# Kernel tuning notes

Hardware: AMD Instinct MI355X
Metric: run time of the kernel (lower is better)

## Reference

```python
import jax, jax.numpy as jnp
import numpy as np

SLOPE = 25.0   # snntorch surrogate.fast_sigmoid default slope
THR = 1.0      # snntorch Leaky default threshold

@jax.custom_vjp
def spike(x):
    # Heaviside forward, fast-sigmoid surrogate backward: g / (slope*|x|+1)^2
    return (x > 0).astype(x.dtype)

def _spike_fwd(x):
    return spike(x), x

def _spike_bwd(x, g):
    return (g / (SLOPE * jnp.abs(x) + 1.0) ** 2,)

spike.defvjp(_spike_fwd, _spike_bwd)

def _lif(mem, cur, beta):
    # snntorch Leaky, reset_mechanism='subtract':
    # reset computed from previous mem (detached), mem = clamp(beta)*mem + cur - reset*thr
    reset = jax.lax.stop_gradient((mem - THR > 0).astype(mem.dtype))
    mem_new = jnp.clip(beta, 0.0, 1.0) * mem + cur - reset * THR
    spk = spike(mem_new - THR)
    return spk, mem_new

def _dsqn_forward(state_batch, hidden_states, W1, b1, beta1, W2, b2, beta2, W3, b3):
    # state_batch: (B, T, F)
    mem1_0 = hidden_states[:, 0, 0, :]  # (B, 128)
    mem2_0 = hidden_states[:, 0, 1, :]
    # layer1 has no recurrence: precompute all timestep currents at once
    cur1_all = jnp.einsum('btf,hf->bth', state_batch, W1) + b1  # (B, T, 128)
    cur1_all = jnp.swapaxes(cur1_all, 0, 1)                     # (T, B, 128)

    def step(carry, cur1):
        mem1, mem2 = carry
        spk1, mem1 = _lif(mem1, cur1, beta1)
        cur2 = spk1 @ W2.T + b2
        spk2, mem2 = _lif(mem2, cur2, beta2)
        out = spk2 @ W3.T + b3
        return (mem1, mem2), out

    _, outs = jax.lax.scan(step, (mem1_0, mem2_0), cur1_all)  # (T, B, A)
    return jnp.swapaxes(outs, 0, 1)  # (B, T, A)

def setup_inputs() -> dict:
    key = jax.random.key(0)
    ks = jax.random.split(key, 10)
    B, T, F, H, A = 512, 1024, 128, 128, 16
    s = 0.05
    return {
        'state_batch': jax.random.normal(ks[0], (B, T, F), jnp.float32),
        'hidden_states': jnp.zeros((B, 1, 2, H), jnp.float32),
        'W1': jax.random.normal(ks[1], (H, F), jnp.float32) * s,
        'b1': jax.random.normal(ks[2], (H,), jnp.float32) * s,
        'beta1': jax.random.uniform(ks[3], (H,), jnp.float32),
        'W2': jax.random.normal(ks[4], (H, H), jnp.float32) * s,
        'b2': jax.random.normal(ks[5], (H,), jnp.float32) * s,
        'beta2': jax.random.uniform(ks[6], (H,), jnp.float32),
        'W3': jax.random.normal(ks[7], (A, H), jnp.float32) * s,
        'b3': jax.random.normal(ks[8], (A,), jnp.float32) * s,
    }

def reference(state_batch, hidden_states, W1, b1, beta1, W2, b2, beta2, W3, b3):
    return _dsqn_forward(state_batch, hidden_states, W1, b1, beta1, W2, b2, beta2, W3, b3)
```

## Files before the change

kernel.cpp:

```cpp
#include <hip/hip_runtime.h>
#include <cstdint>
#include <cstddef>

#define BB 512
#define TT 1024
#define FF 128
#define HH 128
#define AA 16

#define BAR() asm volatile("s_waitcnt lgkmcnt(0)\n\ts_barrier" ::: "memory")

__device__ __forceinline__ float rl(float v, int l) {
    return __int_as_float(__builtin_amdgcn_readlane(__float_as_int(v), l));
}

__global__ __launch_bounds__(512, 4) void dsqn_fused(
    const float* __restrict__ X,
    const float* __restrict__ hid,
    const float* __restrict__ W1,
    const float* __restrict__ b1,
    const float* __restrict__ beta1,
    const float* __restrict__ W2,
    const float* __restrict__ b2,
    const float* __restrict__ beta2,
    const float* __restrict__ W3,
    const float* __restrict__ b3,
    float* __restrict__ out)
{
    __shared__ float p1b[2][4 * HH];
    __shared__ float p2[2 * HH];
    __shared__ float p3b[2][128];
    __shared__ float w3l[128 * 17];
    __shared__ float obuf[8 * AA];

    const int t = threadIdx.x;
    const int b = blockIdx.x;
    const int lane = t & 63;
    const int wid = t >> 6;
    const bool isC2 = (wid < 4);
    const int u = (wid >> 1) & 1;
    const int q = wid & 3;

    float wA[32], wB[32];
    if (isC2) {
        const float* w2p = W2 + (t & 127) * HH + u * 32;
        #pragma unroll
        for (int k = 0; k < 32; ++k) { wA[k] = w2p[k]; wB[k] = w2p[64 + k]; }
    } else {
        const float* wa = W1 + lane * FF + q;
        const float* wb = W1 + (64 + lane) * FF + q;
        #pragma unroll
        for (int k = 0; k < 32; ++k) { wA[k] = wa[4 * k]; wB[k] = wb[4 * k]; }
    }
    for (int i = t; i < 128 * 16; i += 512) {
        const int r = i >> 4, k = i & 15;
        const int a = r & 15, g = r >> 4;
        w3l[r * 17 + k] = W3[a * HH + g * 16 + k];
    }

    float mem1_0 = hid[b * 2 * HH + lane];
    float mem1_1 = hid[b * 2 * HH + 64 + lane];
    float mem2_0 = hid[b * 2 * HH + HH + lane];
    float mem2_1 = hid[b * 2 * HH + HH + 64 + lane];
    const float b1h0 = b1[lane], b1h1 = b1[64 + lane];
    const float bt1_0 = fminf(fmaxf(beta1[lane], 0.f), 1.f);
    const float bt1_1 = fminf(fmaxf(beta1[64 + lane], 0.f), 1.f);
    const float b2j = b2[t & 127];
    const float bt2_0 = fminf(fmaxf(beta2[lane], 0.f), 1.f);
    const float bt2_1 = fminf(fmaxf(beta2[64 + lane], 0.f), 1.f);
    const float b3a = (t < AA) ? b3[t] : 0.f;

    const float* xrow = X + (size_t)b * TT * FF;
    float* orow = out + (size_t)b * TT * AA;

    const int xidx = 4 * (lane & 31) + q;
    float xv = 0.f;

    if (!isC2) {
        const float xv0 = xrow[xidx];
        float a0 = 0.f, a1 = 0.f;
        #pragma unroll
        for (int k = 0; k < 32; ++k) {
            const float xs = rl(xv0, k);
            a0 = fmaf(xs, wA[k], a0);
            a1 = fmaf(xs, wB[k], a1);
        }
        p1b[0][q * 128 + lane] = a0;
        p1b[0][q * 128 + 64 + lane] = a1;
        xv = xrow[FF + xidx];
    }
    BAR();

    for (int st = 0; st < TT; ++st) {
        const int par = st & 1;

        if (isC2) {
            const float* p1c = p1b[par];
            const float c00 = p1c[lane],       c01 = p1c[128 + lane];
            const float c02 = p1c[256 + lane], c03 = p1c[384 + lane];
            const float c10 = p1c[64 + lane],  c11 = p1c[192 + lane];
            const float c12 = p1c[320 + lane], c13 = p1c[448 + lane];
            const float cur1_0 = ((c00 + c01) + (c02 + c03)) + b1h0;
            const float cur1_1 = ((c10 + c11) + (c12 + c13)) + b1h1;
            const float r1_0 = (mem1_0 > 1.0f) ? 1.0f : 0.0f;
            const float r1_1 = (mem1_1 > 1.0f) ? 1.0f : 0.0f;
            mem1_0 = bt1_0 * mem1_0 + cur1_0 - r1_0;
            mem1_1 = bt1_1 * mem1_1 + cur1_1 - r1_1;
            const unsigned long long balA = __ballot((mem1_0 - 1.0f) > 0.0f);
            const unsigned long long balB = __ballot((mem1_1 - 1.0f) > 0.0f);

            const unsigned wlo = u ? (unsigned)(balA >> 32) : (unsigned)balA;
            const unsigned whi = u ? (unsigned)(balB >> 32) : (unsigned)balB;
            const unsigned long long packed =
                (unsigned long long)wlo | ((unsigned long long)whi << 32);
            const unsigned bit = (unsigned)(packed >> lane) & 1u;
            const float mflt = bit ? 1.0f : 0.0f;

            float c = u ? 0.f : b2j;
            #pragma unroll
            for (int k = 0; k < 32; ++k) c = fmaf(rl(mflt, k), wA[k], c);
            #pragma unroll
            for (int k = 0; k < 32; ++k) c = fmaf(rl(mflt, 32 + k), wB[k], c);
            p2[u * 128 + (t & 127)] = c;
        } else {
            float a0 = 0.f, a1 = 0.f;
            #pragma unroll
            for (int k = 0; k < 32; ++k) {
                const float xs = rl(xv, k);
                a0 = fmaf(xs, wA[k], a0);
                a1 = fmaf(xs, wB[k], a1);
            }
            float* p1n = p1b[par ^ 1];
            p1n[q * 128 + lane] = a0;
            p1n[q * 128 + 64 + lane] = a1;
            xv = (st + 2 < TT) ? xrow[2 * FF + xidx] : 0.f;
            xrow += FF;
        }
        BAR();

        if (isC2) {
            const float cur2_0 = p2[lane] + p2[128 + lane];
            const float cur2_1 = p2[64 + lane] + p2[192 + lane];
            const float r2_0 = (mem2_0 > 1.0f) ? 1.0f : 0.0f;
            const float r2_1 = (mem2_1 > 1.0f) ? 1.0f : 0.0f;
            mem2_0 = bt2_0 * mem2_0 + cur2_0 - r2_0;
            mem2_1 = bt2_1 * mem2_1 + cur2_1 - r2_1;
            const unsigned long long balC = __ballot((mem2_0 - 1.0f) > 0.0f);
            const unsigned long long balD = __ballot((mem2_1 - 1.0f) > 0.0f);

            const int r = t & 127;
            const int g = r >> 4;
            const int wi = r >> 5;
            const unsigned w0m = (unsigned)balC, w1m = (unsigned)(balC >> 32);
            const unsigned w2m = (unsigned)balD, w3m = (unsigned)(balD >> 32);
            const unsigned word = (wi == 0) ? w0m : (wi == 1) ? w1m
                                : (wi == 2) ? w2m : w3m;
            const unsigned chunk = (word >> ((g & 1) * 16)) & 0xFFFFu;
            float p = 0.f;
            #pragma unroll
            for (int k = 0; k < 16; ++k) {
                const float m = __uint_as_float(((chunk >> k) & 1u) * 0x3f800000u);
                p = fmaf(m, w3l[r * 17 + k], p);
            }
            p3b[par][r] = p;
        }
        BAR();

        if (t < AA) {
            float o = b3a;
            #pragma unroll
            for (int gg = 0; gg < 8; ++gg) o += p3b[par][gg * 16 + t];
            obuf[(st & 7) * AA + t] = o;
        }
        if ((st & 7) == 7) {
            BAR();
            if (t < 128) orow[(st - 7) * AA + t] = obuf[t];
        }
    }
}

extern "C" void kernel_launch(void* const* d_in, const int* in_sizes, int n_in,
                              void* d_out, int out_size, void* d_ws, size_t ws_size,
                              hipStream_t stream) {
    const float* X     = (const float*)d_in[0];
    const float* hid   = (const float*)d_in[1];
    const float* W1    = (const float*)d_in[2];
    const float* b1    = (const float*)d_in[3];
    const float* beta1 = (const float*)d_in[4];
    const float* W2    = (const float*)d_in[5];
    const float* b2    = (const float*)d_in[6];
    const float* beta2 = (const float*)d_in[7];
    const float* W3    = (const float*)d_in[8];
    const float* b3    = (const float*)d_in[9];
    float* out = (float*)d_out;

    dsqn_fused<<<BB, 512, 0, stream>>>(X, hid, W1, b1, beta1, W2, b2, beta2, W3, b3, out);
}
```

Measured before the change: 1.718 ms.

## Move layer-3 projection to layer-1 waves, pipelined one step behind, drop barrier

The layer-3 matvec moves from the layer-2 waves to the otherwise idle layer-1 waves. It runs one timestep late, reading spike masks that are published to LDS as four words, and uses W3 held in registers. This removes the third barrier per step and the extra barrier every eighth step. Outputs are now written straight to global memory each step instead of going through an 8-step LDS buffer, and the final step is finished in an epilogue. The cost is more per-step work on the layer-1 waves, more register pressure there, and narrower global stores.

```diff
diff --git a/kernel.cpp b/kernel.cpp
--- a/kernel.cpp
+++ b/kernel.cpp
@@ -9,6 +9,8 @@
 #define AA 16
 
 #define BAR() asm volatile("s_waitcnt lgkmcnt(0)\n\ts_barrier" ::: "memory")
+
+typedef float f32x2 __attribute__((ext_vector_type(2)));
 
 __device__ __forceinline__ float rl(float v, int l) {
     return __int_as_float(__builtin_amdgcn_readlane(__float_as_int(v), l));
@@ -29,9 +31,8 @@
 {
     __shared__ float p1b[2][4 * HH];
     __shared__ float p2[2 * HH];
-    __shared__ float p3b[2][128];
-    __shared__ float w3l[128 * 17];
-    __shared__ float obuf[8 * AA];
+    __shared__ float p3[128];
+    __shared__ unsigned mw2s[4];
 
     const int t = threadIdx.x;
     const int b = blockIdx.x;
@@ -41,40 +42,53 @@
     const int u = (wid >> 1) & 1;
     const int q = wid & 3;
 
-    float wA[32], wB[32];
+    f32x2 wv[32];
+    float w3r[16];
+    int r3 = 0;
     if (isC2) {
         const float* w2p = W2 + (t & 127) * HH + u * 32;
         #pragma unroll
-        for (int k = 0; k < 32; ++k) { wA[k] = w2p[k]; wB[k] = w2p[64 + k]; }
+        for (int k = 0; k < 32; ++k) { wv[k].x = w2p[k]; wv[k].y = w2p[64 + k]; }
     } else {
         const float* wa = W1 + lane * FF + q;
         const float* wb = W1 + (64 + lane) * FF + q;
         #pragma unroll
-        for (int k = 0; k < 32; ++k) { wA[k] = wa[4 * k]; wB[k] = wb[4 * k]; }
-    }
-    for (int i = t; i < 128 * 16; i += 512) {
-        const int r = i >> 4, k = i & 15;
-        const int a = r & 15, g = r >> 4;
-        w3l[r * 17 + k] = W3[a * HH + g * 16 + k];
-    }
-
-    float mem1_0 = hid[b * 2 * HH + lane];
-    float mem1_1 = hid[b * 2 * HH + 64 + lane];
-    float mem2_0 = hid[b * 2 * HH + HH + lane];
-    float mem2_1 = hid[b * 2 * HH + HH + 64 + lane];
-    const float b1h0 = b1[lane], b1h1 = b1[64 + lane];
-    const float bt1_0 = fminf(fmaxf(beta1[lane], 0.f), 1.f);
-    const float bt1_1 = fminf(fmaxf(beta1[64 + lane], 0.f), 1.f);
-    const float b2j = b2[t & 127];
-    const float bt2_0 = fminf(fmaxf(beta2[lane], 0.f), 1.f);
-    const float bt2_1 = fminf(fmaxf(beta2[64 + lane], 0.f), 1.f);
-    const float b3a = (t < AA) ? b3[t] : 0.f;
+        for (int k = 0; k < 32; ++k) { wv[k].x = wa[4 * k]; wv[k].y = wb[4 * k]; }
+        r3 = ((wid & 1) << 6) | lane;
+        const int a3 = r3 & 15, g3 = r3 >> 4;
+        const float* w3p = W3 + a3 * HH + g3 * 16;
+        #pragma unroll
+        for (int k = 0; k < 16; ++k) w3r[k] = w3p[k];
+        #pragma unroll
+        for (int k = 0; k < 16; ++k) asm volatile("" : "+v"(w3r[k]));
+    }
+    #pragma unroll
+    for (int k = 0; k < 32; ++k) asm volatile("" : "+v"(wv[k]));
+
+    float mem1_0 = 0.f, mem1_1 = 0.f, mem2_0 = 0.f, mem2_1 = 0.f;
+    float b1h0 = 0.f, b1h1 = 0.f, bt1_0 = 0.f, bt1_1 = 0.f;
+    float b2j = 0.f, bt2_0 = 0.f, bt2_1 = 0.f;
+    if (isC2) {
+        mem1_0 = hid[b * 2 * HH + lane];
+        mem1_1 = hid[b * 2 * HH + 64 + lane];
+        mem2_0 = hid[b * 2 * HH + HH + lane];
+        mem2_1 = hid[b * 2 * HH + HH + 64 + lane];
+        b1h0 = b1[lane]; b1h1 = b1[64 + lane];
+        bt1_0 = fminf(fmaxf(beta1[lane], 0.f), 1.f);
+        bt1_1 = fminf(fmaxf(beta1[64 + lane], 0.f), 1.f);
+        b2j = b2[t & 127];
+        bt2_0 = fminf(fmaxf(beta2[lane], 0.f), 1.f);
+        bt2_1 = fminf(fmaxf(beta2[64 + lane], 0.f), 1.f);
+    }
+    float b3a = 0.f;
+    if (wid == 4) b3a = b3[lane & 15];
 
     const float* xrow = X + (size_t)b * TT * FF;
     float* orow = out + (size_t)b * TT * AA;
-
     const int xidx = 4 * (lane & 31) + q;
     float xv = 0.f;
+
+    if (t == 0) { mw2s[0] = 0u; mw2s[1] = 0u; mw2s[2] = 0u; mw2s[3] = 0u; }
 
     if (!isC2) {
         const float xv0 = xrow[xidx];
@@ -82,8 +96,8 @@
         #pragma unroll
         for (int k = 0; k < 32; ++k) {
             const float xs = rl(xv0, k);
-            a0 = fmaf(xs, wA[k], a0);
-            a1 = fmaf(xs, wB[k], a1);
+            a0 = fmaf(xs, wv[k].x, a0);
+            a1 = fmaf(xs, wv[k].y, a1);
         }
         p1b[0][q * 128 + lane] = a0;
         p1b[0][q * 128 + 64 + lane] = a1;
@@ -113,26 +127,42 @@
             const unsigned whi = u ? (unsigned)(balB >> 32) : (unsigned)balB;
             const unsigned long long packed =
                 (unsigned long long)wlo | ((unsigned long long)whi << 32);
-            const unsigned bit = (unsigned)(packed >> lane) & 1u;
-            const float mflt = bit ? 1.0f : 0.0f;
+            const float mflt = ((unsigned)(packed >> lane) & 1u) ? 1.0f : 0.0f;
 
             float c = u ? 0.f : b2j;
             #pragma unroll
-            for (int k = 0; k < 32; ++k) c = fmaf(rl(mflt, k), wA[k], c);
-            #pragma unroll
-            for (int k = 0; k < 32; ++k) c = fmaf(rl(mflt, 32 + k), wB[k], c);
+            for (int k = 0; k < 32; ++k) c = fmaf(rl(mflt, k), wv[k].x, c);
+            #pragma unroll
+            for (int k = 0; k < 32; ++k) c = fmaf(rl(mflt, 32 + k), wv[k].y, c);
             p2[u * 128 + (t & 127)] = c;
         } else {
             float a0 = 0.f, a1 = 0.f;
             #pragma unroll
             for (int k = 0; k < 32; ++k) {
                 const float xs = rl(xv, k);
-                a0 = fmaf(xs, wA[k], a0);
-                a1 = fmaf(xs, wB[k], a1);
+                a0 = fmaf(xs, wv[k].x, a0);
+                a1 = fmaf(xs, wv[k].y, a1);
             }
             float* p1n = p1b[par ^ 1];
             p1n[q * 128 + lane] = a0;
             p1n[q * 128 + 64 + lane] = a1;
+
+            {
+                const unsigned w0m = mw2s[0], w1m = mw2s[1];
+                const unsigned w2m = mw2s[2], w3m = mw2s[3];
+                const int g = r3 >> 4;
+                const int wi = r3 >> 5;
+                const unsigned word = (wi == 0) ? w0m : (wi == 1) ? w1m
+                                    : (wi == 2) ? w2m : w3m;
+                const unsigned chunk = (word >> ((g & 1) * 16)) & 0xFFFFu;
+                float p = 0.f;
+                #pragma unroll
+                for (int k = 0; k < 16; ++k) {
+                    const float m = ((chunk >> k) & 1u) ? 1.0f : 0.0f;
+                    p = fmaf(m, w3r[k], p);
+                }
+                p3[r3] = p;
+            }
             xv = (st + 2 < TT) ? xrow[2 * FF + xidx] : 0.f;
             xrow += FF;
         }
@@ -147,35 +177,41 @@
             mem2_1 = bt2_1 * mem2_1 + cur2_1 - r2_1;
             const unsigned long long balC = __ballot((mem2_0 - 1.0f) > 0.0f);
             const unsigned long long balD = __ballot((mem2_1 - 1.0f) > 0.0f);
-
-            const int r = t & 127;
-            const int g = r >> 4;
-            const int wi = r >> 5;
-            const unsigned w0m = (unsigned)balC, w1m = (unsigned)(balC >> 32);
-            const unsigned w2m = (unsigned)balD, w3m = (unsigned)(balD >> 32);
-            const unsigned word = (wi == 0) ? w0m : (wi == 1) ? w1m
-                                : (wi == 2) ? w2m : w3m;
-            const unsigned chunk = (word >> ((g & 1) * 16)) & 0xFFFFu;
-            float p = 0.f;
-            #pragma unroll
-            for (int k = 0; k < 16; ++k) {
-                const float m = __uint_as_float(((chunk >> k) & 1u) * 0x3f800000u);
-                p = fmaf(m, w3l[r * 17 + k], p);
+            if (t == 0) {
+                mw2s[0] = (unsigned)balC; mw2s[1] = (unsigned)(balC >> 32);
+                mw2s[2] = (unsigned)balD; mw2s[3] = (unsigned)(balD >> 32);
             }
-            p3b[par][r] = p;
+        } else if (wid == 4 && lane < AA && st) {
+            float o = b3a;
+            #pragma unroll
+            for (int gg = 0; gg < 8; ++gg) o += p3[gg * 16 + lane];
+            orow[(st - 1) * AA + lane] = o;
         }
         BAR();
-
-        if (t < AA) {
-            float o = b3a;
-            #pragma unroll
-            for (int gg = 0; gg < 8; ++gg) o += p3b[par][gg * 16 + t];
-            obuf[(st & 7) * AA + t] = o;
-        }
-        if ((st & 7) == 7) {
-            BAR();
-            if (t < 128) orow[(st - 7) * AA + t] = obuf[t];
-        }
+    }
+
+    if (!isC2) {
+        const unsigned w0m = mw2s[0], w1m = mw2s[1];
+        const unsigned w2m = mw2s[2], w3m = mw2s[3];
+        const int g = r3 >> 4;
+        const int wi = r3 >> 5;
+        const unsigned word = (wi == 0) ? w0m : (wi == 1) ? w1m
+                            : (wi == 2) ? w2m : w3m;
+        const unsigned chunk = (word >> ((g & 1) * 16)) & 0xFFFFu;
+        float p = 0.f;
+        #pragma unroll
+        for (int k = 0; k < 16; ++k) {
+            const float m = ((chunk >> k) & 1u) ? 1.0f : 0.0f;
+            p = fmaf(m, w3r[k], p);
+        }
+        p3[r3] = p;
+    }
+    BAR();
+    if (wid == 4 && lane < AA) {
+        float o = b3a;
+        #pragma unroll
+        for (int gg = 0; gg < 8; ++gg) o += p3[gg * 16 + lane];
+        orow[(TT - 1) * AA + lane] = o;
     }
 }
 
```

Result: slower. 1.809 ms (+5.3%).
